# Optimization experiments

Measured on AMD Instinct MI355X. Metric: run time of the kernel, lower is better.

Reference implementation:

```python
import jax, jax.numpy as jnp
import numpy as np
from jax import lax

VOC = 32000; H = 512; T = 256; B = 64; L = 2; MAXLEN = 32; SOS = 1


def setup_inputs() -> dict:
    key = jax.random.key(0)
    ks = jax.random.split(key, 20)
    s = 1.0 / np.sqrt(H)
    u = lambda k, shape: jax.random.uniform(k, shape, jnp.float32, -s, s)
    inp = {}
    inp["input"] = jax.random.randint(ks[0], (T, B), 0, VOC)
    inp["emb_enc"] = jax.random.normal(ks[1], (VOC, H), jnp.float32) * 0.1
    inp["emb_dec"] = jax.random.normal(ks[2], (VOC, H), jnp.float32) * 0.1
    # GRU weights, torch layout: W_ih (3H, in), W_hh (3H, H), biases (3H,); stacked over layers
    inp["enc_Wih"] = u(ks[3], (L, 3 * H, H)); inp["enc_Whh"] = u(ks[4], (L, 3 * H, H))
    inp["enc_bih"] = u(ks[5], (L, 3 * H));   inp["enc_bhh"] = u(ks[6], (L, 3 * H))
    inp["dec_Wih"] = u(ks[7], (L, 3 * H, H)); inp["dec_Whh"] = u(ks[8], (L, 3 * H, H))
    inp["dec_bih"] = u(ks[9], (L, 3 * H));   inp["dec_bhh"] = u(ks[10], (L, 3 * H))
    inp["attn_W"] = u(ks[11], (T, (L + 1) * H)); inp["attn_b"] = u(ks[12], (T,))
    inp["comb_W"] = u(ks[13], (H, 2 * H));       inp["comb_b"] = u(ks[14], (H,))
    inp["avg_W"] = u(ks[15], (1, H))   # dueling value head, no bias
    inp["adv_W"] = u(ks[16], (VOC, H)) # dueling advantage head, no bias
    return inp


def _gru_cell(x, h, Wih, Whh, bih, bhh):
    gi = x @ Wih.T + bih
    gh = h @ Whh.T + bhh
    ir, iz, in_ = jnp.split(gi, 3, axis=-1)
    hr, hz, hn = jnp.split(gh, 3, axis=-1)
    r = jax.nn.sigmoid(ir + hr)
    z = jax.nn.sigmoid(iz + hz)
    n = jnp.tanh(in_ + r * hn)
    return (1.0 - z) * n + z * h


def _gru_step(x, h, Wih, Whh, bih, bhh):
    # x: (B,H), h: (L,B,H) -> new h (L,B,H), top-layer output (B,H)
    hs = []
    for l in range(L):
        hl = _gru_cell(x, h[l], Wih[l], Whh[l], bih[l], bhh[l])
        hs.append(hl)
        x = hl
    return jnp.stack(hs), x


def _forward(input, emb_enc, emb_dec, enc_Wih, enc_Whh, enc_bih, enc_bhh,
             dec_Wih, dec_Whh, dec_bih, dec_bhh, attn_W, attn_b,
             comb_W, comb_b, avg_W, adv_W):
    # ----- encoder -----
    emb = jax.nn.relu(emb_enc[input])  # (T,B,H)
    h0 = jnp.zeros((L, B, H), jnp.float32)

    def enc_step(h, x):
        h2, top = _gru_step(x, h, enc_Wih, enc_Whh, enc_bih, enc_bhh)
        return h2, top

    states, gru_out = lax.scan(enc_step, h0, emb)  # gru_out: (T,B,H)

    def dec_step(carry, _):
        h, word = carry
        e = jax.nn.relu(emb_dec[word])                       # (B,H)
        sv = jnp.reshape(h, (B, L * H))                      # matches torch .view(-1,1,L*H)
        a = jax.nn.relu(jnp.concatenate([e, sv], -1) @ attn_W.T + attn_b)  # (B,T)
        applied = jnp.einsum('bt,tbh->bh', a, gru_out)       # (B,H)
        comb = jax.nn.relu(jnp.concatenate([e, applied], -1) @ comb_W.T + comb_b)
        h2, top = _gru_step(comb, h, dec_Wih, dec_Whh, dec_bih, dec_bhh)
        values = top @ avg_W.T + top @ adv_W.T               # (B,1)+(B,VOC) -> (B,VOC)
        word2 = jnp.argmax(values, axis=-1)
        q = jnp.take_along_axis(values, word2[:, None], axis=-1)[:, 0]
        return (h2, word2), (top, q)

    word0 = jnp.full((B,), SOS, dtype=jnp.int32)
    _, (tops, qs) = lax.scan(dec_step, (states, word0), None, length=MAXLEN)
    sentences = tops[:, None]  # (MAXLEN,1,B,H) mirrors stacking (1,B,H) rnn_outs
    return sentences, qs       # qs: (MAXLEN,B)


def reference(input, emb_enc, emb_dec, enc_Wih, enc_Whh, enc_bih, enc_bhh,
              dec_Wih, dec_Whh, dec_bih, dec_bhh, attn_W, attn_b,
              comb_W, comb_b, avg_W, adv_W):
    return _forward(input, emb_enc, emb_dec, enc_Wih, enc_Whh, enc_bih, enc_bhh,
                    dec_Wih, dec_Whh, dec_bih, dec_bhh, attn_W, attn_b,
                    comb_W, comb_b, avg_W, adv_W)
```

## Files before the change

### kernel.cpp

```cpp
#include <hip/hip_runtime.h>
#include <math.h>

#define VOCN 32000
#define HN 512
#define TN 256
#define BN 64
#define MAXLENN 32
#define SOSW 1

#define WS_FLAG     0
#define WS_REL      8192
#define WS_H        8448
#define WS_WORD     (WS_H + 131072)
#define WS_A        (WS_WORD + 64)
#define WS_APPLIED  (WS_A + 16384)
#define WS_COMB     (WS_APPLIED + 32768)
#define WS_PVAL     (WS_COMB + 32768)
#define WS_PIDX     (WS_PVAL + 16384)
#define WS_GRUOUT   (WS_PIDX + 16384)
#define WS_ZERO_BYTES ((WS_H + 131072) * 4)

typedef float f4 __attribute__((ext_vector_type(4)));

__device__ __forceinline__ f4 ld4(const float* p) { return *(const f4*)p; }
__device__ __forceinline__ float dot4(f4 a, f4 b, float acc) {
  acc = fmaf(a.x, b.x, acc); acc = fmaf(a.y, b.y, acc);
  acc = fmaf(a.z, b.z, acc); acc = fmaf(a.w, b.w, acc); return acc;
}
__device__ __forceinline__ f4 relu4(f4 v) {
  v.x = fmaxf(v.x, 0.f); v.y = fmaxf(v.y, 0.f);
  v.z = fmaxf(v.z, 0.f); v.w = fmaxf(v.w, 0.f); return v;
}
__device__ __forceinline__ float sigmoidf_(float x) { return 1.f / (1.f + expf(-x)); }

__device__ __forceinline__ float ldcg(const float* p) {
  float v;
  asm volatile("global_load_dword %0, %1, off sc0 sc1\n\ts_waitcnt vmcnt(0)"
               : "=&v"(v) : "v"(p) : "memory");
  return v;
}
__device__ __forceinline__ int ldcg_i(const int* p) {
  int v;
  asm volatile("global_load_dword %0, %1, off sc0 sc1\n\ts_waitcnt vmcnt(0)"
               : "=&v"(v) : "v"(p) : "memory");
  return v;
}
__device__ __forceinline__ void stcg(float* p, float v) {
  asm volatile("global_store_dword %0, %1, off sc0 sc1" :: "v"(p), "v"(v) : "memory");
}
__device__ __forceinline__ void stcg_i(int* p, int v) {
  asm volatile("global_store_dword %0, %1, off sc0 sc1" :: "v"(p), "v"(v) : "memory");
}
__device__ __forceinline__ void ldcg_b4(const float* p0, const float* p1,
                                        const float* p2, const float* p3,
                                        f4& v0, f4& v1, f4& v2, f4& v3) {
  asm volatile(
      "global_load_dwordx4 %0, %4, off sc0 sc1\n\t"
      "global_load_dwordx4 %1, %5, off sc0 sc1\n\t"
      "global_load_dwordx4 %2, %6, off sc0 sc1\n\t"
      "global_load_dwordx4 %3, %7, off sc0 sc1\n\t"
      "s_waitcnt vmcnt(0)"
      : "=&v"(v0), "=&v"(v1), "=&v"(v2), "=&v"(v3)
      : "v"(p0), "v"(p1), "v"(p2), "v"(p3)
      : "memory");
}
__device__ __forceinline__ void ldcg_b8(const float* p0, const float* p1,
    const float* p2, const float* p3, const float* p4, const float* p5,
    const float* p6, const float* p7,
    f4& v0, f4& v1, f4& v2, f4& v3, f4& v4, f4& v5, f4& v6, f4& v7) {
  asm volatile(
      "global_load_dwordx4 %0, %8, off sc0 sc1\n\t"
      "global_load_dwordx4 %1, %9, off sc0 sc1\n\t"
      "global_load_dwordx4 %2, %10, off sc0 sc1\n\t"
      "global_load_dwordx4 %3, %11, off sc0 sc1\n\t"
      "global_load_dwordx4 %4, %12, off sc0 sc1\n\t"
      "global_load_dwordx4 %5, %13, off sc0 sc1\n\t"
      "global_load_dwordx4 %6, %14, off sc0 sc1\n\t"
      "global_load_dwordx4 %7, %15, off sc0 sc1\n\t"
      "s_waitcnt vmcnt(0)"
      : "=&v"(v0), "=&v"(v1), "=&v"(v2), "=&v"(v3),
        "=&v"(v4), "=&v"(v5), "=&v"(v6), "=&v"(v7)
      : "v"(p0), "v"(p1), "v"(p2), "v"(p3), "v"(p4), "v"(p5), "v"(p6), "v"(p7)
      : "memory");
}
__device__ __forceinline__ void ldcg_row8(const float* p, f4 (&v)[8]) {
  asm volatile(
      "global_load_dwordx4 %0, %8, off sc0 sc1\n\t"
      "global_load_dwordx4 %1, %8, off offset:16 sc0 sc1\n\t"
      "global_load_dwordx4 %2, %8, off offset:32 sc0 sc1\n\t"
      "global_load_dwordx4 %3, %8, off offset:48 sc0 sc1\n\t"
      "global_load_dwordx4 %4, %8, off offset:64 sc0 sc1\n\t"
      "global_load_dwordx4 %5, %8, off offset:80 sc0 sc1\n\t"
      "global_load_dwordx4 %6, %8, off offset:96 sc0 sc1\n\t"
      "global_load_dwordx4 %7, %8, off offset:112 sc0 sc1\n\t"
      "s_waitcnt vmcnt(0)"
      : "=&v"(v[0]), "=&v"(v[1]), "=&v"(v[2]), "=&v"(v[3]),
        "=&v"(v[4]), "=&v"(v[5]), "=&v"(v[6]), "=&v"(v[7])
      : "v"(p)
      : "memory");
}

__device__ __forceinline__ void grid_barrier(int* wsi, int gen) {
  asm volatile("s_waitcnt vmcnt(0) lgkmcnt(0)" ::: "memory");
  __syncthreads();
  const int bid = blockIdx.x;
  const int tid = threadIdx.x;
  if (bid == 0) {
    if (tid == 0)
      __hip_atomic_store(wsi + WS_FLAG, gen, __ATOMIC_RELAXED, __HIP_MEMORY_SCOPE_AGENT);
    int* fp = wsi + WS_FLAG + tid * 32;
    for (;;) {
      int v = __hip_atomic_load(fp, __ATOMIC_RELAXED, __HIP_MEMORY_SCOPE_AGENT);
      if (__syncthreads_and(v >= gen)) break;
      __builtin_amdgcn_s_sleep(2);
    }
    if (tid < 8)
      __hip_atomic_store(wsi + WS_REL + tid * 16, gen, __ATOMIC_RELAXED, __HIP_MEMORY_SCOPE_AGENT);
    __syncthreads();
  } else {
    if (tid == 0) {
      __hip_atomic_store(wsi + WS_FLAG + bid * 32, gen, __ATOMIC_RELAXED, __HIP_MEMORY_SCOPE_AGENT);
      int* rp = wsi + WS_REL + (bid & 7) * 16;
      while (__hip_atomic_load(rp, __ATOMIC_RELAXED, __HIP_MEMORY_SCOPE_AGENT) < gen)
        __builtin_amdgcn_s_sleep(2);
    }
    __syncthreads();
  }
}

__device__ __forceinline__ void gru_phase(
    const float* __restrict__ x_base, const int* __restrict__ tok,
    const float* __restrict__ h_rows,
    const float* __restrict__ Wih, const float* __restrict__ Whh,
    const float* __restrict__ bih, const float* __restrict__ bhh,
    float* __restrict__ h_out, float* __restrict__ aux_out,
    int rb, float* lds)
{
  const int tid = threadIdx.x;
  const int bg = rb >> 6;
  const int jg = rb & 63;
  f4* x4l = (f4*)lds;
  f4* h4l = ((f4*)lds) + 1024;

  const float* xp[4]; const float* hp[4]; int loff[4];
#pragma unroll
  for (int i = 0; i < 4; ++i) {
    int tau = tid + (i << 8);
    int b = tau >> 5;
    int kq = tau & 31;
    int gb = bg * 32 + b;
    const float* xr = tok ? (x_base + (size_t)tok[gb] * HN) : (x_base + (size_t)gb * HN);
    xp[i] = xr + (kq << 2);
    hp[i] = h_rows + (size_t)gb * HN + (kq << 2);
    loff[i] = (b << 5) + (kq ^ (b & 7));
  }
  const bool cachedx = (tok != nullptr);
  f4 pxv[4], phv[4];
  if (cachedx) {
#pragma unroll
    for (int i = 0; i < 4; ++i) pxv[i] = ld4(xp[i]);
    ldcg_b4(hp[0], hp[1], hp[2], hp[3], phv[0], phv[1], phv[2], phv[3]);
  } else {
    ldcg_b8(xp[0], xp[1], xp[2], xp[3], hp[0], hp[1], hp[2], hp[3],
            pxv[0], pxv[1], pxv[2], pxv[3], phv[0], phv[1], phv[2], phv[3]);
  }

  const int bl = tid & 31;
  const int jl = tid >> 5;
  const int j = (jg << 3) + jl;
  const float* wi0 = Wih + (size_t)j * HN;
  const float* wi1 = Wih + (size_t)(512 + j) * HN;
  const float* wi2 = Wih + (size_t)(1024 + j) * HN;
  const float* wh0 = Whh + (size_t)j * HN;
  const float* wh1 = Whh + (size_t)(512 + j) * HN;
  const float* wh2 = Whh + (size_t)(1024 + j) * HN;
  float ax0 = 0.f, ax1 = 0.f, ax2 = 0.f, ah0 = 0.f, ah1 = 0.f, ah2 = 0.f;
  const int rdbase = bl << 5;
  const int rdx = bl & 7;

#pragma unroll 1
  for (int ch = 0; ch < 4; ++ch) {
    __syncthreads();
#pragma unroll
    for (int i = 0; i < 4; ++i) {
      x4l[loff[i]] = cachedx ? relu4(pxv[i]) : pxv[i];
      h4l[loff[i]] = phv[i];
    }
    __syncthreads();
    if (ch < 3) {
      const int off = (ch + 1) * 128;
      if (cachedx) {
#pragma unroll
        for (int i = 0; i < 4; ++i) pxv[i] = ld4(xp[i] + off);
        ldcg_b4(hp[0] + off, hp[1] + off, hp[2] + off, hp[3] + off,
                phv[0], phv[1], phv[2], phv[3]);
      } else {
        ldcg_b8(xp[0] + off, xp[1] + off, xp[2] + off, xp[3] + off,
                hp[0] + off, hp[1] + off, hp[2] + off, hp[3] + off,
                pxv[0], pxv[1], pxv[2], pxv[3], phv[0], phv[1], phv[2], phv[3]);
      }
    }
    const int k0 = ch << 7;
#pragma unroll 4
    for (int kq = 0; kq < 32; ++kq) {
      f4 xv = x4l[rdbase + (kq ^ rdx)];
      f4 hv = h4l[rdbase + (kq ^ rdx)];
      const int kk = k0 + (kq << 2);
      ax0 = dot4(xv, ld4(wi0 + kk), ax0);
      ah0 = dot4(hv, ld4(wh0 + kk), ah0);
      ax1 = dot4(xv, ld4(wi1 + kk), ax1);
      ah1 = dot4(hv, ld4(wh1 + kk), ah1);
      ax2 = dot4(xv, ld4(wi2 + kk), ax2);
      ah2 = dot4(hv, ld4(wh2 + kk), ah2);
    }
  }
  const int gb = bg * 32 + bl;
  const float hold = ldcg(h_rows + (size_t)gb * HN + j);
  const float r = sigmoidf_(ax0 + bih[j] + ah0 + bhh[j]);
  const float z = sigmoidf_(ax1 + bih[512 + j] + ah1 + bhh[512 + j]);
  const float n = tanhf(ax2 + bih[1024 + j] + r * (ah2 + bhh[1024 + j]));
  const float hv = (1.f - z) * n + z * hold;
  stcg(h_out + (size_t)gb * HN + j, hv);
  if (aux_out) stcg(aux_out + (size_t)gb * HN + j, hv);
}

__device__ __forceinline__ void d1_attn(
    const float* __restrict__ emb_dec, const int* __restrict__ word_buf, int s,
    const float* __restrict__ hflat, const float* __restrict__ attn_W,
    const float* __restrict__ attn_b, float* __restrict__ a_buf, int bid, float* lds)
{
  const int tid = threadIdx.x;
  const int b = tid & 63, q = tid >> 6;
  int wb = (s == 0) ? SOSW : ldcg_i(word_buf + b);
  wb = wb < 0 ? 0 : (wb > VOCN - 1 ? VOCN - 1 : wb);
  const float* er = emb_dec + (size_t)wb * HN;
  const float* hr = hflat + b * 1024;
  const float* wr = attn_W + (size_t)bid * 1536;
  float acc = 0.f;
  const int kbeg = q * 384, kend = kbeg + 384;
  int k = kbeg;
  const int kc = (kend < 512) ? kend : 512;
  for (; k < kc; k += 4)
    acc = dot4(relu4(ld4(er + k)), ld4(wr + k), acc);
  if (k < 512) k = 512;
  for (; k < kend; k += 32) {
    f4 hv[8]; ldcg_row8(hr + (k - 512), hv);
#pragma unroll
    for (int jq = 0; jq < 8; ++jq)
      acc = dot4(hv[jq], ld4(wr + k + (jq << 2)), acc);
  }
  lds[(b << 2) + q] = acc;
  __syncthreads();
  if (tid < 64) {
    float v = lds[tid * 4] + lds[tid * 4 + 1] + lds[tid * 4 + 2] + lds[tid * 4 + 3];
    v += attn_b[bid];
    stcg(a_buf + tid * 256 + bid, fmaxf(v, 0.f));
  }
}

__device__ __forceinline__ void d2_applied(const float* __restrict__ a_buf,
    const float* __restrict__ gru_out, float* __restrict__ applied, int bid, float* lds)
{
  const int tid = threadIdx.x;
  const int b = bid & 63, hc = bid >> 6;
  f4* al4 = (f4*)lds;
  float* al = lds;
  float* red = lds + 256;
  if (tid < 64) {
    f4 av;
    const float* p = a_buf + b * 256 + (tid << 2);
    asm volatile("global_load_dwordx4 %0, %1, off sc0 sc1\n\ts_waitcnt vmcnt(0)"
                 : "=&v"(av) : "v"(p) : "memory");
    al4[tid] = av;
  }
  __syncthreads();
  const int hl = tid & 127, th = tid >> 7;
  const int hh = (hc << 7) + hl;
  const float* gp = gru_out + (size_t)b * HN + hh;
  float acc = 0.f;
  const int t0 = th << 7;
#pragma unroll 4
  for (int t = t0; t < t0 + 128; ++t)
    acc = fmaf(al[t], gp[(size_t)t * (BN * HN)], acc);
  red[tid] = acc;
  __syncthreads();
  if (tid < 128)
    stcg(applied + (size_t)b * HN + (hc << 7) + tid, red[tid] + red[tid + 128]);
}

__device__ __forceinline__ void d3_comb(const float* __restrict__ emb_dec,
    const int* __restrict__ word_buf, int s, const float* __restrict__ applied,
    const float* __restrict__ comb_W, const float* __restrict__ comb_b,
    float* __restrict__ comb, int bid, float* lds)
{
  const int tid = threadIdx.x;
  const int b = tid & 63, q = tid >> 6;
  int wb = (s == 0) ? SOSW : ldcg_i(word_buf + b);
  wb = wb < 0 ? 0 : (wb > VOCN - 1 ? VOCN - 1 : wb);
  const float* er = emb_dec + (size_t)wb * HN;
  const float* apr = applied + (size_t)b * HN;
#pragma unroll
  for (int cc = 0; cc < 2; ++cc) {
    const int col = (bid << 1) + cc;
    const float* wr = comb_W + (size_t)col * 1024;
    float acc = 0.f;
    const int kbeg = q << 8, kend = kbeg + 256;
    int k = kbeg;
    const int kc = (kend < 512) ? kend : 512;
    for (; k < kc; k += 4)
      acc = dot4(relu4(ld4(er + k)), ld4(wr + k), acc);
    if (k < 512) k = 512;
    for (; k < kend; k += 32) {
      f4 av[8]; ldcg_row8(apr + (k - 512), av);
#pragma unroll
      for (int jq = 0; jq < 8; ++jq)
        acc = dot4(av[jq], ld4(wr + k + (jq << 2)), acc);
    }
    lds[cc * 256 + (b << 2) + q] = acc;
  }
  __syncthreads();
  if (tid < 128) {
    const int cc = tid >> 6, b2 = tid & 63;
    const int col = (bid << 1) + cc;
    float v = lds[cc * 256 + b2 * 4] + lds[cc * 256 + b2 * 4 + 1] +
              lds[cc * 256 + b2 * 4 + 2] + lds[cc * 256 + b2 * 4 + 3];
    v += comb_b[col];
    stcg(comb + (size_t)b2 * HN + col, fmaxf(v, 0.f));
  }
}

__device__ __forceinline__ void d6_values(const float* __restrict__ top,
    const float* __restrict__ adv_W, float* __restrict__ pval, int* __restrict__ pidx,
    int bid, float* lds)
{
  const int tid = threadIdx.x;
  const int c0 = bid * 125;
  f4* tl = (f4*)lds;
  f4* wl = ((f4*)lds) + 2048;
  float* sval = lds + 12288;
  int* sidx = (int*)(lds + 12288 + 256);

  const float* tp[8]; int loff[8];
#pragma unroll
  for (int i = 0; i < 8; ++i) {
    int tau = tid + (i << 8);
    int b = tau >> 5, kq = tau & 31;
    tp[i] = top + b * HN + (kq << 2);
    loff[i] = (b << 5) + (kq ^ (b & 7));
  }
  f4 pv[8];
  ldcg_b8(tp[0], tp[1], tp[2], tp[3], tp[4], tp[5], tp[6], tp[7],
          pv[0], pv[1], pv[2], pv[3], pv[4], pv[5], pv[6], pv[7]);

  const int bl = tid & 63;
  const int cq = tid >> 6;
  const int rdbase = bl << 5;
  const int rdx = bl & 7;

  float acc[32];
#pragma unroll
  for (int i = 0; i < 32; ++i) acc[i] = 0.f;

#pragma unroll 1
  for (int ch = 0; ch < 4; ++ch) {
    __syncthreads();
#pragma unroll
    for (int i = 0; i < 8; ++i) tl[loff[i]] = pv[i];
    __syncthreads();
    if (ch < 3) {
      const int off = (ch + 1) * 128;
      ldcg_b8(tp[0] + off, tp[1] + off, tp[2] + off, tp[3] + off,
              tp[4] + off, tp[5] + off, tp[6] + off, tp[7] + off,
              pv[0], pv[1], pv[2], pv[3], pv[4], pv[5], pv[6], pv[7]);
    }
#pragma unroll 1
    for (int cg = 0; cg < 4; ++cg) {
#pragma unroll
      for (int r = 0; r < 4; ++r) {
        const int qq = tid + (r << 8);
        int c = c0 + (cg << 5) + (qq >> 5);
        if (c > VOCN - 1) c = VOCN - 1;
        wl[qq] = ld4(adv_W + (size_t)c * HN + (ch << 7) + ((qq & 31) << 2));
      }
      __syncthreads();
      const int wbase = cq << 8;
#pragma unroll 4
      for (int kq = 0; kq < 32; ++kq) {
        f4 tv = tl[rdbase + (kq ^ rdx)];
        const int wq = wbase + kq;
        acc[(cg << 3) + 0] = dot4(tv, wl[wq +   0], acc[(cg << 3) + 0]);
        acc[(cg << 3) + 1] = dot4(tv, wl[wq +  32], acc[(cg << 3) + 1]);
        acc[(cg << 3) + 2] = dot4(tv, wl[wq +  64], acc[(cg << 3) + 2]);
        acc[(cg << 3) + 3] = dot4(tv, wl[wq +  96], acc[(cg << 3) + 3]);
        acc[(cg << 3) + 4] = dot4(tv, wl[wq + 128], acc[(cg << 3) + 4]);
        acc[(cg << 3) + 5] = dot4(tv, wl[wq + 160], acc[(cg << 3) + 5]);
        acc[(cg << 3) + 6] = dot4(tv, wl[wq + 192], acc[(cg << 3) + 6]);
        acc[(cg << 3) + 7] = dot4(tv, wl[wq + 224], acc[(cg << 3) + 7]);
      }
      __syncthreads();
    }
  }
  float bv = -3.4e38f; int bi = 2147483647;
#pragma unroll
  for (int i = 0; i < 32; ++i) {
    const int cl = ((i >> 3) << 5) + (cq << 3) + (i & 7);
    if (cl < 125) {
      float v = acc[i];
      if (v > bv) { bv = v; bi = c0 + cl; }
    }
  }
  sval[(bl << 2) + cq] = bv;
  sidx[(bl << 2) + cq] = bi;
  __syncthreads();
  if (tid < 64) {
    float v = sval[tid << 2]; int ii = sidx[tid << 2];
#pragma unroll
    for (int h2 = 1; h2 < 4; ++h2) {
      float v2 = sval[(tid << 2) + h2]; int i2 = sidx[(tid << 2) + h2];
      if (v2 > v || (v2 == v && i2 < ii)) { v = v2; ii = i2; }
    }
    stcg(pval + tid * 256 + bid, v);
    stcg_i(pidx + tid * 256 + bid, ii);
  }
}

__device__ __forceinline__ void d7_reduce(const float* __restrict__ top,
    const float* __restrict__ avg_W, const float* __restrict__ pval,
    const int* __restrict__ pidx, float* __restrict__ qs_out,
    int* __restrict__ word_buf, float* lds)
{
  const int tid = threadIdx.x;
  const int b = tid & 63, q = tid >> 6;
  const float* tr = top + (size_t)b * HN;
  float p = 0.f;
  const int kbeg = q << 7;
#pragma unroll
  for (int bb = 0; bb < 4; ++bb) {
    f4 tv[8]; ldcg_row8(tr + kbeg + bb * 32, tv);
#pragma unroll
    for (int jq = 0; jq < 8; ++jq)
      p = dot4(tv[jq], ld4(avg_W + kbeg + bb * 32 + (jq << 2)), p);
  }
  float* av = lds;
  float* avl = lds + 256;
  float* rv = lds + 320;
  int* ri = (int*)(lds + 576);
  av[(b << 2) + q] = p;
  __syncthreads();
  if (tid < 64)
    avl[tid] = av[tid * 4] + av[tid * 4 + 1] + av[tid * 4 + 2] + av[tid * 4 + 3];
  float bv = -3.4e38f; int bi = 2147483647;
  const float* pvr = pval + b * 256 + (q << 6);
  const float* pir = (const float*)(pidx) + b * 256 + (q << 6);
#pragma unroll
  for (int bb = 0; bb < 2; ++bb) {
    f4 v4[8], i4[8];
    ldcg_row8(pvr + bb * 32, v4);
    ldcg_row8(pir + bb * 32, i4);
#pragma unroll
    for (int jq = 0; jq < 8; ++jq) {
      float vv[4] = { v4[jq].x, v4[jq].y, v4[jq].z, v4[jq].w };
      int iv[4] = { __float_as_int(i4[jq].x), __float_as_int(i4[jq].y),
                    __float_as_int(i4[jq].z), __float_as_int(i4[jq].w) };
#pragma unroll
      for (int c = 0; c < 4; ++c) {
        if (vv[c] > bv || (vv[c] == bv && iv[c] < bi)) { bv = vv[c]; bi = iv[c]; }
      }
    }
  }
  rv[(b << 2) + q] = bv;
  ri[(b << 2) + q] = bi;
  __syncthreads();
  if (tid < 64) {
    float v = rv[tid << 2]; int ii = ri[tid << 2];
#pragma unroll
    for (int k = 1; k < 4; ++k) {
      float v2 = rv[(tid << 2) + k]; int i2 = ri[(tid << 2) + k];
      if (v2 > v || (v2 == v && i2 < ii)) { v = v2; ii = i2; }
    }
    qs_out[tid] = v + avl[tid];
    stcg_i(word_buf + tid, ii);
  }
}

__global__ void __launch_bounds__(256)
seq2seq_kernel(const int* __restrict__ input, const float* __restrict__ emb_enc,
               const float* __restrict__ emb_dec,
               const float* __restrict__ enc_Wih, const float* __restrict__ enc_Whh,
               const float* __restrict__ enc_bih, const float* __restrict__ enc_bhh,
               const float* __restrict__ dec_Wih, const float* __restrict__ dec_Whh,
               const float* __restrict__ dec_bih, const float* __restrict__ dec_bhh,
               const float* __restrict__ attn_W, const float* __restrict__ attn_b,
               const float* __restrict__ comb_W, const float* __restrict__ comb_b,
               const float* __restrict__ avg_W, const float* __restrict__ adv_W,
               float* __restrict__ out, float* __restrict__ ws)
{
  __shared__ float lds[12800];
  const int bid = blockIdx.x;
  int* wsi = (int*)ws;
  float* hbuf = ws + WS_H;
  int* word_buf = (int*)(ws + WS_WORD);
  float* a_buf = ws + WS_A;
  float* applied = ws + WS_APPLIED;
  float* comb = ws + WS_COMB;
  float* pval = ws + WS_PVAL;
  int* pidx = (int*)(ws + WS_PIDX);
  float* gru_out = ws + WS_GRUOUT;
  int gen = 0;

#pragma unroll 1
  for (int p = 0; p <= 256; ++p) {
    if (bid < 128) {
      if (p < 256) {
        const int t = p;
        gru_phase(emb_enc, input + t * BN,
                  hbuf + (size_t)(t & 1) * 65536,
                  enc_Wih, enc_Whh, enc_bih, enc_bhh,
                  hbuf + (size_t)((t + 1) & 1) * 65536,
                  nullptr, bid, lds);
      }
    } else {
      if (p >= 1) {
        const int t = p - 1;
        gru_phase(hbuf + (size_t)((t + 1) & 1) * 65536, nullptr,
                  hbuf + (size_t)(t & 1) * 65536 + 32768,
                  enc_Wih + 786432, enc_Whh + 786432,
                  enc_bih + 1536, enc_bhh + 1536,
                  hbuf + (size_t)((t + 1) & 1) * 65536 + 32768,
                  gru_out + (size_t)t * (BN * HN), bid - 128, lds);
      }
    }
    grid_barrier(wsi, ++gen);
  }

  __threadfence();

#pragma unroll 1
  for (int s = 0; s < 32; ++s) {
    const float* hflat = hbuf + (size_t)(s & 1) * 65536;
    float* hnew = hbuf + (size_t)((s + 1) & 1) * 65536;

    d1_attn(emb_dec, word_buf, s, hflat, attn_W, attn_b, a_buf, bid, lds);
    grid_barrier(wsi, ++gen);

    d2_applied(a_buf, gru_out, applied, bid, lds);
    grid_barrier(wsi, ++gen);

    d3_comb(emb_dec, word_buf, s, applied, comb_W, comb_b, comb, bid, lds);
    grid_barrier(wsi, ++gen);

    if (bid < 128)
      gru_phase(comb, nullptr, hflat, dec_Wih, dec_Whh, dec_bih, dec_bhh,
                hnew, nullptr, bid, lds);
    grid_barrier(wsi, ++gen);

    if (bid < 128)
      gru_phase(hnew, nullptr, hflat + 32768,
                dec_Wih + 786432, dec_Whh + 786432, dec_bih + 1536, dec_bhh + 1536,
                hnew + 32768, out + (size_t)s * (BN * HN), bid, lds);
    grid_barrier(wsi, ++gen);

    d6_values(hnew + 32768, adv_W, pval, pidx, bid, lds);
    grid_barrier(wsi, ++gen);

    if (bid == 0)
      d7_reduce(hnew + 32768, avg_W, pval, pidx,
                out + (size_t)MAXLENN * BN * HN + s * BN, word_buf, lds);
    grid_barrier(wsi, ++gen);
  }
}

extern "C" void kernel_launch(void* const* d_in, const int* in_sizes, int n_in,
                              void* d_out, int out_size, void* d_ws, size_t ws_size,
                              hipStream_t stream) {
  (void)in_sizes; (void)n_in; (void)out_size; (void)ws_size;
  const int* input      = (const int*)d_in[0];
  const float* emb_enc  = (const float*)d_in[1];
  const float* emb_dec  = (const float*)d_in[2];
  const float* enc_Wih  = (const float*)d_in[3];
  const float* enc_Whh  = (const float*)d_in[4];
  const float* enc_bih  = (const float*)d_in[5];
  const float* enc_bhh  = (const float*)d_in[6];
  const float* dec_Wih  = (const float*)d_in[7];
  const float* dec_Whh  = (const float*)d_in[8];
  const float* dec_bih  = (const float*)d_in[9];
  const float* dec_bhh  = (const float*)d_in[10];
  const float* attn_W   = (const float*)d_in[11];
  const float* attn_b   = (const float*)d_in[12];
  const float* comb_W   = (const float*)d_in[13];
  const float* comb_b   = (const float*)d_in[14];
  const float* avg_W    = (const float*)d_in[15];
  const float* adv_W    = (const float*)d_in[16];
  float* out = (float*)d_out;
  float* ws  = (float*)d_ws;

  hipMemsetAsync(d_ws, 0, WS_ZERO_BYTES, stream);

  seq2seq_kernel<<<dim3(256), dim3(256), 0, stream>>>(
      input, emb_enc, emb_dec, enc_Wih, enc_Whh, enc_bih, enc_bhh,
      dec_Wih, dec_Whh, dec_bih, dec_bhh, attn_W, attn_b,
      comb_W, comb_b, avg_W, adv_W, out, ws);
}
```

Before: 21.47 ms.

## Replace argmax reduce phase with packed 64-bit atomic max and double block size

Drops the separate single-block argmax reduction phase and its grid barrier. Each decoder step's per-block argmax is now merged through a 64-bit atomic max on order-preserving float keys with an inverted index for ties, and the word and q-value are decoded in the next step. Blocks grow to 512 threads, so the GRU phases run on half as many blocks with two batch groups each, and the attention, applied, comb and value phases are reorganised for the wider block, with the avg-head dot moved into block 0 of the value phase. This cuts 32 grid barriers and a serial reduction, at the cost of global atomics, larger LDS use and possible occupancy changes.

```diff
diff --git a/kernel.cpp b/kernel.cpp
--- a/kernel.cpp
+++ b/kernel.cpp
@@ -11,14 +11,13 @@
 #define WS_FLAG     0
 #define WS_REL      8192
 #define WS_H        8448
-#define WS_WORD     (WS_H + 131072)
-#define WS_A        (WS_WORD + 64)
+#define WS_CELLS    (WS_H + 131072)
+#define WS_AVG      (WS_CELLS + 4096)
+#define WS_A        (WS_AVG + 64)
 #define WS_APPLIED  (WS_A + 16384)
 #define WS_COMB     (WS_APPLIED + 32768)
-#define WS_PVAL     (WS_COMB + 32768)
-#define WS_PIDX     (WS_PVAL + 16384)
-#define WS_GRUOUT   (WS_PIDX + 16384)
-#define WS_ZERO_BYTES ((WS_H + 131072) * 4)
+#define WS_GRUOUT   (WS_COMB + 32768)
+#define WS_ZERO_BYTES ((WS_CELLS + 4096) * 4)
 
 typedef float f4 __attribute__((ext_vector_type(4)));
 
@@ -39,16 +38,7 @@
                : "=&v"(v) : "v"(p) : "memory");
   return v;
 }
-__device__ __forceinline__ int ldcg_i(const int* p) {
-  int v;
-  asm volatile("global_load_dword %0, %1, off sc0 sc1\n\ts_waitcnt vmcnt(0)"
-               : "=&v"(v) : "v"(p) : "memory");
-  return v;
-}
 __device__ __forceinline__ void stcg(float* p, float v) {
-  asm volatile("global_store_dword %0, %1, off sc0 sc1" :: "v"(p), "v"(v) : "memory");
-}
-__device__ __forceinline__ void stcg_i(int* p, int v) {
   asm volatile("global_store_dword %0, %1, off sc0 sc1" :: "v"(p), "v"(v) : "memory");
 }
 __device__ __forceinline__ void ldcg_b4(const float* p0, const float* p1,
@@ -108,9 +98,11 @@
   if (bid == 0) {
     if (tid == 0)
       __hip_atomic_store(wsi + WS_FLAG, gen, __ATOMIC_RELAXED, __HIP_MEMORY_SCOPE_AGENT);
-    int* fp = wsi + WS_FLAG + tid * 32;
+    int* fp = wsi + WS_FLAG + (tid & 255) * 32;
     for (;;) {
-      int v = __hip_atomic_load(fp, __ATOMIC_RELAXED, __HIP_MEMORY_SCOPE_AGENT);
+      int v = gen;
+      if (tid < 256)
+        v = __hip_atomic_load(fp, __ATOMIC_RELAXED, __HIP_MEMORY_SCOPE_AGENT);
       if (__syncthreads_and(v >= gen)) break;
       __builtin_amdgcn_s_sleep(2);
     }
@@ -128,24 +120,39 @@
   }
 }
 
+__device__ __forceinline__ unsigned ord_enc(float v) {
+  unsigned u = __float_as_uint(v);
+  return (u & 0x80000000u) ? ~u : (u | 0x80000000u);
+}
+__device__ __forceinline__ float ord_dec(unsigned k32) {
+  unsigned u = (k32 & 0x80000000u) ? (k32 ^ 0x80000000u) : ~k32;
+  return __uint_as_float(u);
+}
+__device__ __forceinline__ int decode_word(const unsigned long long* cell) {
+  unsigned long long key = __hip_atomic_load(cell, __ATOMIC_RELAXED,
+                                             __HIP_MEMORY_SCOPE_AGENT);
+  int wb = (int)(0xFFFFFFFFu - (unsigned)(key & 0xFFFFFFFFull));
+  return wb < 0 ? 0 : (wb > VOCN - 1 ? VOCN - 1 : wb);
+}
+
 __device__ __forceinline__ void gru_phase(
     const float* __restrict__ x_base, const int* __restrict__ tok,
     const float* __restrict__ h_rows,
     const float* __restrict__ Wih, const float* __restrict__ Whh,
     const float* __restrict__ bih, const float* __restrict__ bhh,
     float* __restrict__ h_out, float* __restrict__ aux_out,
-    int rb, float* lds)
+    int jg, float* lds)
 {
   const int tid = threadIdx.x;
-  const int bg = rb >> 6;
-  const int jg = rb & 63;
-  f4* x4l = (f4*)lds;
-  f4* h4l = ((f4*)lds) + 1024;
+  const int tid2 = tid & 255;
+  const int bg = tid >> 8;
+  f4* x4l = (f4*)lds + (bg << 11);
+  f4* h4l = x4l + 1024;
 
   const float* xp[4]; const float* hp[4]; int loff[4];
 #pragma unroll
   for (int i = 0; i < 4; ++i) {
-    int tau = tid + (i << 8);
+    int tau = tid2 + (i << 8);
     int b = tau >> 5;
     int kq = tau & 31;
     int gb = bg * 32 + b;
@@ -165,8 +172,8 @@
             pxv[0], pxv[1], pxv[2], pxv[3], phv[0], phv[1], phv[2], phv[3]);
   }
 
-  const int bl = tid & 31;
-  const int jl = tid >> 5;
+  const int bl = tid2 & 31;
+  const int jl = tid2 >> 5;
   const int j = (jg << 3) + jl;
   const float* wi0 = Wih + (size_t)j * HN;
   const float* wi1 = Wih + (size_t)(512 + j) * HN;
@@ -225,19 +232,29 @@
 }
 
 __device__ __forceinline__ void d1_attn(
-    const float* __restrict__ emb_dec, const int* __restrict__ word_buf, int s,
-    const float* __restrict__ hflat, const float* __restrict__ attn_W,
-    const float* __restrict__ attn_b, float* __restrict__ a_buf, int bid, float* lds)
+    const float* __restrict__ emb_dec, const unsigned long long* __restrict__ cells,
+    int s, const float* __restrict__ hflat, const float* __restrict__ attn_W,
+    const float* __restrict__ attn_b, float* __restrict__ a_buf,
+    const float* __restrict__ avg_buf, float* __restrict__ qs_base,
+    int bid, float* lds)
 {
   const int tid = threadIdx.x;
   const int b = tid & 63, q = tid >> 6;
-  int wb = (s == 0) ? SOSW : ldcg_i(word_buf + b);
-  wb = wb < 0 ? 0 : (wb > VOCN - 1 ? VOCN - 1 : wb);
+  int* wlds = (int*)(lds + 576);
+  if (s > 0 && tid < 64)
+    wlds[tid] = decode_word(cells + (size_t)(s - 1) * 64 + tid);
+  if (s > 0 && bid == 0 && tid < 64) {
+    unsigned long long key = __hip_atomic_load(cells + (size_t)(s - 1) * 64 + tid,
+                                               __ATOMIC_RELAXED, __HIP_MEMORY_SCOPE_AGENT);
+    qs_base[(size_t)(s - 1) * BN + tid] = ord_dec((unsigned)(key >> 32)) + ldcg(avg_buf + tid);
+  }
+  __syncthreads();
+  const int wb = (s == 0) ? SOSW : wlds[b];
   const float* er = emb_dec + (size_t)wb * HN;
   const float* hr = hflat + b * 1024;
   const float* wr = attn_W + (size_t)bid * 1536;
   float acc = 0.f;
-  const int kbeg = q * 384, kend = kbeg + 384;
+  const int kbeg = q * 192, kend = kbeg + 192;
   int k = kbeg;
   const int kc = (kend < 512) ? kend : 512;
   for (; k < kc; k += 4)
@@ -249,10 +266,13 @@
     for (int jq = 0; jq < 8; ++jq)
       acc = dot4(hv[jq], ld4(wr + k + (jq << 2)), acc);
   }
-  lds[(b << 2) + q] = acc;
+  __syncthreads();
+  lds[(b << 3) + q] = acc;
   __syncthreads();
   if (tid < 64) {
-    float v = lds[tid * 4] + lds[tid * 4 + 1] + lds[tid * 4 + 2] + lds[tid * 4 + 3];
+    float v = 0.f;
+#pragma unroll
+    for (int i = 0; i < 8; ++i) v += lds[(tid << 3) + i];
     v += attn_b[bid];
     stcg(a_buf + tid * 256 + bid, fmaxf(v, 0.f));
   }
@@ -278,212 +298,172 @@
   const int hh = (hc << 7) + hl;
   const float* gp = gru_out + (size_t)b * HN + hh;
   float acc = 0.f;
-  const int t0 = th << 7;
+  const int t0 = th << 6;
 #pragma unroll 4
-  for (int t = t0; t < t0 + 128; ++t)
+  for (int t = t0; t < t0 + 64; ++t)
     acc = fmaf(al[t], gp[(size_t)t * (BN * HN)], acc);
   red[tid] = acc;
   __syncthreads();
   if (tid < 128)
-    stcg(applied + (size_t)b * HN + (hc << 7) + tid, red[tid] + red[tid + 128]);
+    stcg(applied + (size_t)b * HN + (hc << 7) + tid,
+         red[tid] + red[tid + 128] + red[tid + 256] + red[tid + 384]);
 }
 
 __device__ __forceinline__ void d3_comb(const float* __restrict__ emb_dec,
-    const int* __restrict__ word_buf, int s, const float* __restrict__ applied,
-    const float* __restrict__ comb_W, const float* __restrict__ comb_b,
-    float* __restrict__ comb, int bid, float* lds)
+    const unsigned long long* __restrict__ cells, int s,
+    const float* __restrict__ applied, const float* __restrict__ comb_W,
+    const float* __restrict__ comb_b, float* __restrict__ comb, int bid, float* lds)
 {
   const int tid = threadIdx.x;
   const int b = tid & 63, q = tid >> 6;
-  int wb = (s == 0) ? SOSW : ldcg_i(word_buf + b);
-  wb = wb < 0 ? 0 : (wb > VOCN - 1 ? VOCN - 1 : wb);
+  int* wlds = (int*)(lds + 1088);
+  if (s > 0 && tid < 64)
+    wlds[tid] = decode_word(cells + (size_t)(s - 1) * 64 + tid);
+  __syncthreads();
+  const int wb = (s == 0) ? SOSW : wlds[b];
   const float* er = emb_dec + (size_t)wb * HN;
   const float* apr = applied + (size_t)b * HN;
-#pragma unroll
-  for (int cc = 0; cc < 2; ++cc) {
-    const int col = (bid << 1) + cc;
-    const float* wr = comb_W + (size_t)col * 1024;
-    float acc = 0.f;
-    const int kbeg = q << 8, kend = kbeg + 256;
-    int k = kbeg;
-    const int kc = (kend < 512) ? kend : 512;
-    for (; k < kc; k += 4)
-      acc = dot4(relu4(ld4(er + k)), ld4(wr + k), acc);
-    if (k < 512) k = 512;
-    for (; k < kend; k += 32) {
-      f4 av[8]; ldcg_row8(apr + (k - 512), av);
-#pragma unroll
-      for (int jq = 0; jq < 8; ++jq)
-        acc = dot4(av[jq], ld4(wr + k + (jq << 2)), acc);
-    }
-    lds[cc * 256 + (b << 2) + q] = acc;
-  }
+  const int col0 = bid << 1;
+  const float* w0 = comb_W + (size_t)col0 * 1024;
+  const float* w1 = w0 + 1024;
+  float a0 = 0.f, a1 = 0.f;
+  const int kb = q << 7;
+  if (q < 4) {
+    for (int k = kb; k < kb + 128; k += 4) {
+      f4 e = relu4(ld4(er + k));
+      a0 = dot4(e, ld4(w0 + k), a0);
+      a1 = dot4(e, ld4(w1 + k), a1);
+    }
+  } else {
+#pragma unroll 1
+    for (int r = 0; r < 4; ++r) {
+      f4 av[8]; ldcg_row8(apr + (kb - 512) + (r << 5), av);
+#pragma unroll
+      for (int jq = 0; jq < 8; ++jq) {
+        a0 = dot4(av[jq], ld4(w0 + kb + (r << 5) + (jq << 2)), a0);
+        a1 = dot4(av[jq], ld4(w1 + kb + (r << 5) + (jq << 2)), a1);
+      }
+    }
+  }
+  __syncthreads();
+  lds[(b << 3) + q] = a0;
+  lds[512 + (b << 3) + q] = a1;
   __syncthreads();
   if (tid < 128) {
     const int cc = tid >> 6, b2 = tid & 63;
-    const int col = (bid << 1) + cc;
-    float v = lds[cc * 256 + b2 * 4] + lds[cc * 256 + b2 * 4 + 1] +
-              lds[cc * 256 + b2 * 4 + 2] + lds[cc * 256 + b2 * 4 + 3];
-    v += comb_b[col];
-    stcg(comb + (size_t)b2 * HN + col, fmaxf(v, 0.f));
+    const float* base = lds + cc * 512;
+    float v = 0.f;
+#pragma unroll
+    for (int i = 0; i < 8; ++i) v += base[(b2 << 3) + i];
+    v += comb_b[col0 + cc];
+    stcg(comb + (size_t)b2 * HN + col0 + cc, fmaxf(v, 0.f));
   }
 }
 
 __device__ __forceinline__ void d6_values(const float* __restrict__ top,
-    const float* __restrict__ adv_W, float* __restrict__ pval, int* __restrict__ pidx,
+    const float* __restrict__ adv_W, const float* __restrict__ avg_W,
+    unsigned long long* __restrict__ cellsS, float* __restrict__ avg_buf,
     int bid, float* lds)
 {
   const int tid = threadIdx.x;
   const int c0 = bid * 125;
   f4* tl = (f4*)lds;
   f4* wl = ((f4*)lds) + 2048;
-  float* sval = lds + 12288;
-  int* sidx = (int*)(lds + 12288 + 256);
-
-  const float* tp[8]; int loff[8];
-#pragma unroll
-  for (int i = 0; i < 8; ++i) {
-    int tau = tid + (i << 8);
+
+  const float* tp[4]; int loff[4];
+#pragma unroll
+  for (int i = 0; i < 4; ++i) {
+    int tau = tid + (i << 9);
     int b = tau >> 5, kq = tau & 31;
     tp[i] = top + b * HN + (kq << 2);
     loff[i] = (b << 5) + (kq ^ (b & 7));
   }
-  f4 pv[8];
-  ldcg_b8(tp[0], tp[1], tp[2], tp[3], tp[4], tp[5], tp[6], tp[7],
-          pv[0], pv[1], pv[2], pv[3], pv[4], pv[5], pv[6], pv[7]);
-
-  const int bl = tid & 63;
-  const int cq = tid >> 6;
-  const int rdbase = bl << 5;
-  const int rdx = bl & 7;
-
-  float acc[32];
-#pragma unroll
-  for (int i = 0; i < 32; ++i) acc[i] = 0.f;
+  f4 pv[4];
+  ldcg_b4(tp[0], tp[1], tp[2], tp[3], pv[0], pv[1], pv[2], pv[3]);
+
+  const int rp = tid >> 4;
+  const int co = tid & 15;
+  const int r0 = rp << 1;
+  float acc0[8], acc1[8];
+#pragma unroll
+  for (int i = 0; i < 8; ++i) { acc0[i] = 0.f; acc1[i] = 0.f; }
+  float avgacc = 0.f;
 
 #pragma unroll 1
   for (int ch = 0; ch < 4; ++ch) {
     __syncthreads();
 #pragma unroll
-    for (int i = 0; i < 8; ++i) tl[loff[i]] = pv[i];
+    for (int i = 0; i < 4; ++i) tl[loff[i]] = pv[i];
     __syncthreads();
     if (ch < 3) {
       const int off = (ch + 1) * 128;
-      ldcg_b8(tp[0] + off, tp[1] + off, tp[2] + off, tp[3] + off,
-              tp[4] + off, tp[5] + off, tp[6] + off, tp[7] + off,
-              pv[0], pv[1], pv[2], pv[3], pv[4], pv[5], pv[6], pv[7]);
+      ldcg_b4(tp[0] + off, tp[1] + off, tp[2] + off, tp[3] + off,
+              pv[0], pv[1], pv[2], pv[3]);
+    }
+    if (bid == 0 && tid < 64) {
+#pragma unroll 4
+      for (int kq = 0; kq < 32; ++kq)
+        avgacc = dot4(tl[(tid << 5) + (kq ^ (tid & 7))],
+                      ld4(avg_W + (ch << 7) + (kq << 2)), avgacc);
     }
 #pragma unroll 1
-    for (int cg = 0; cg < 4; ++cg) {
+    for (int w = 0; w < 2; ++w) {
 #pragma unroll
       for (int r = 0; r < 4; ++r) {
-        const int qq = tid + (r << 8);
-        int c = c0 + (cg << 5) + (qq >> 5);
-        if (c > VOCN - 1) c = VOCN - 1;
-        wl[qq] = ld4(adv_W + (size_t)c * HN + (ch << 7) + ((qq & 31) << 2));
+        const int qq = tid + (r << 9);
+        const int cl = qq >> 4, kql = qq & 15;
+        int c = c0 + cl; if (c > VOCN - 1) c = VOCN - 1;
+        wl[(cl << 4) + (kql ^ ((cl >> 3) & 7))] =
+            ld4(adv_W + (size_t)c * HN + (ch << 7) + (w << 6) + (kql << 2));
       }
       __syncthreads();
-      const int wbase = cq << 8;
-#pragma unroll 4
-      for (int kq = 0; kq < 32; ++kq) {
-        f4 tv = tl[rdbase + (kq ^ rdx)];
-        const int wq = wbase + kq;
-        acc[(cg << 3) + 0] = dot4(tv, wl[wq +   0], acc[(cg << 3) + 0]);
-        acc[(cg << 3) + 1] = dot4(tv, wl[wq +  32], acc[(cg << 3) + 1]);
-        acc[(cg << 3) + 2] = dot4(tv, wl[wq +  64], acc[(cg << 3) + 2]);
-        acc[(cg << 3) + 3] = dot4(tv, wl[wq +  96], acc[(cg << 3) + 3]);
-        acc[(cg << 3) + 4] = dot4(tv, wl[wq + 128], acc[(cg << 3) + 4]);
-        acc[(cg << 3) + 5] = dot4(tv, wl[wq + 160], acc[(cg << 3) + 5]);
-        acc[(cg << 3) + 6] = dot4(tv, wl[wq + 192], acc[(cg << 3) + 6]);
-        acc[(cg << 3) + 7] = dot4(tv, wl[wq + 224], acc[(cg << 3) + 7]);
+      const int kqb = w << 4;
+#pragma unroll 2
+      for (int kql = 0; kql < 16; ++kql) {
+        const int kq = kqb + kql;
+        f4 t0 = tl[(r0 << 5) + (kq ^ (r0 & 7))];
+        f4 t1 = tl[((r0 + 1) << 5) + (kq ^ ((r0 + 1) & 7))];
+#pragma unroll
+        for (int j = 0; j < 8; ++j) {
+          const int cl = (co << 3) + j;
+          f4 wv = wl[(cl << 4) + (kql ^ ((cl >> 3) & 7))];
+          acc0[j] = dot4(t0, wv, acc0[j]);
+          acc1[j] = dot4(t1, wv, acc1[j]);
+        }
       }
       __syncthreads();
     }
   }
-  float bv = -3.4e38f; int bi = 2147483647;
-#pragma unroll
-  for (int i = 0; i < 32; ++i) {
-    const int cl = ((i >> 3) << 5) + (cq << 3) + (i & 7);
+  float bv0 = -3.4e38f, bv1 = -3.4e38f; int bi0 = 2147483647, bi1 = 2147483647;
+#pragma unroll
+  for (int j = 0; j < 8; ++j) {
+    const int cl = (co << 3) + j;
     if (cl < 125) {
-      float v = acc[i];
-      if (v > bv) { bv = v; bi = c0 + cl; }
-    }
-  }
-  sval[(bl << 2) + cq] = bv;
-  sidx[(bl << 2) + cq] = bi;
+      if (acc0[j] > bv0) { bv0 = acc0[j]; bi0 = c0 + cl; }
+      if (acc1[j] > bv1) { bv1 = acc1[j]; bi1 = c0 + cl; }
+    }
+  }
+  float* sval = lds;
+  int* sidx = (int*)(lds + 1024);
+  sval[(r0 << 4) + co] = bv0;  sidx[(r0 << 4) + co] = bi0;
+  sval[((r0 + 1) << 4) + co] = bv1;  sidx[((r0 + 1) << 4) + co] = bi1;
   __syncthreads();
   if (tid < 64) {
-    float v = sval[tid << 2]; int ii = sidx[tid << 2];
-#pragma unroll
-    for (int h2 = 1; h2 < 4; ++h2) {
-      float v2 = sval[(tid << 2) + h2]; int i2 = sidx[(tid << 2) + h2];
+    float v = sval[tid << 4]; int ii = sidx[tid << 4];
+#pragma unroll
+    for (int h2 = 1; h2 < 16; ++h2) {
+      float v2 = sval[(tid << 4) + h2]; int i2 = sidx[(tid << 4) + h2];
       if (v2 > v || (v2 == v && i2 < ii)) { v = v2; ii = i2; }
     }
-    stcg(pval + tid * 256 + bid, v);
-    stcg_i(pidx + tid * 256 + bid, ii);
-  }
-}
-
-__device__ __forceinline__ void d7_reduce(const float* __restrict__ top,
-    const float* __restrict__ avg_W, const float* __restrict__ pval,
-    const int* __restrict__ pidx, float* __restrict__ qs_out,
-    int* __restrict__ word_buf, float* lds)
-{
-  const int tid = threadIdx.x;
-  const int b = tid & 63, q = tid >> 6;
-  const float* tr = top + (size_t)b * HN;
-  float p = 0.f;
-  const int kbeg = q << 7;
-#pragma unroll
-  for (int bb = 0; bb < 4; ++bb) {
-    f4 tv[8]; ldcg_row8(tr + kbeg + bb * 32, tv);
-#pragma unroll
-    for (int jq = 0; jq < 8; ++jq)
-      p = dot4(tv[jq], ld4(avg_W + kbeg + bb * 32 + (jq << 2)), p);
-  }
-  float* av = lds;
-  float* avl = lds + 256;
-  float* rv = lds + 320;
-  int* ri = (int*)(lds + 576);
-  av[(b << 2) + q] = p;
-  __syncthreads();
-  if (tid < 64)
-    avl[tid] = av[tid * 4] + av[tid * 4 + 1] + av[tid * 4 + 2] + av[tid * 4 + 3];
-  float bv = -3.4e38f; int bi = 2147483647;
-  const float* pvr = pval + b * 256 + (q << 6);
-  const float* pir = (const float*)(pidx) + b * 256 + (q << 6);
-#pragma unroll
-  for (int bb = 0; bb < 2; ++bb) {
-    f4 v4[8], i4[8];
-    ldcg_row8(pvr + bb * 32, v4);
-    ldcg_row8(pir + bb * 32, i4);
-#pragma unroll
-    for (int jq = 0; jq < 8; ++jq) {
-      float vv[4] = { v4[jq].x, v4[jq].y, v4[jq].z, v4[jq].w };
-      int iv[4] = { __float_as_int(i4[jq].x), __float_as_int(i4[jq].y),
-                    __float_as_int(i4[jq].z), __float_as_int(i4[jq].w) };
-#pragma unroll
-      for (int c = 0; c < 4; ++c) {
-        if (vv[c] > bv || (vv[c] == bv && iv[c] < bi)) { bv = vv[c]; bi = iv[c]; }
-      }
-    }
-  }
-  rv[(b << 2) + q] = bv;
-  ri[(b << 2) + q] = bi;
-  __syncthreads();
-  if (tid < 64) {
-    float v = rv[tid << 2]; int ii = ri[tid << 2];
-#pragma unroll
-    for (int k = 1; k < 4; ++k) {
-      float v2 = rv[(tid << 2) + k]; int i2 = ri[(tid << 2) + k];
-      if (v2 > v || (v2 == v && i2 < ii)) { v = v2; ii = i2; }
-    }
-    qs_out[tid] = v + avl[tid];
-    stcg_i(word_buf + tid, ii);
-  }
-}
-
-__global__ void __launch_bounds__(256)
+    unsigned long long key = ((unsigned long long)ord_enc(v) << 32) |
+                             (unsigned long long)(0xFFFFFFFFu - (unsigned)ii);
+    __hip_atomic_fetch_max(cellsS + tid, key, __ATOMIC_RELAXED,
+                           __HIP_MEMORY_SCOPE_AGENT);
+  }
+  if (bid == 0 && tid < 64) stcg(avg_buf + tid, avgacc);
+}
+
+__global__ void __launch_bounds__(512)
 seq2seq_kernel(const int* __restrict__ input, const float* __restrict__ emb_enc,
                const float* __restrict__ emb_dec,
                const float* __restrict__ enc_Wih, const float* __restrict__ enc_Whh,
@@ -495,31 +475,30 @@
                const float* __restrict__ avg_W, const float* __restrict__ adv_W,
                float* __restrict__ out, float* __restrict__ ws)
 {
-  __shared__ float lds[12800];
+  __shared__ float lds[16384];
   const int bid = blockIdx.x;
   int* wsi = (int*)ws;
   float* hbuf = ws + WS_H;
-  int* word_buf = (int*)(ws + WS_WORD);
+  unsigned long long* cells = (unsigned long long*)(ws + WS_CELLS);
+  float* avg_buf = ws + WS_AVG;
   float* a_buf = ws + WS_A;
   float* applied = ws + WS_APPLIED;
   float* comb = ws + WS_COMB;
-  float* pval = ws + WS_PVAL;
-  int* pidx = (int*)(ws + WS_PIDX);
   float* gru_out = ws + WS_GRUOUT;
+  float* qs_base = out + (size_t)MAXLENN * BN * HN;
   int gen = 0;
 
 #pragma unroll 1
   for (int p = 0; p <= 256; ++p) {
-    if (bid < 128) {
+    if (bid < 64) {
       if (p < 256) {
-        const int t = p;
-        gru_phase(emb_enc, input + t * BN,
-                  hbuf + (size_t)(t & 1) * 65536,
+        gru_phase(emb_enc, input + p * BN,
+                  hbuf + (size_t)(p & 1) * 65536,
                   enc_Wih, enc_Whh, enc_bih, enc_bhh,
-                  hbuf + (size_t)((t + 1) & 1) * 65536,
+                  hbuf + (size_t)((p + 1) & 1) * 65536,
                   nullptr, bid, lds);
       }
-    } else {
+    } else if (bid < 128) {
       if (p >= 1) {
         const int t = p - 1;
         gru_phase(hbuf + (size_t)((t + 1) & 1) * 65536, nullptr,
@@ -527,7 +506,7 @@
                   enc_Wih + 786432, enc_Whh + 786432,
                   enc_bih + 1536, enc_bhh + 1536,
                   hbuf + (size_t)((t + 1) & 1) * 65536 + 32768,
-                  gru_out + (size_t)t * (BN * HN), bid - 128, lds);
+                  gru_out + (size_t)t * (BN * HN), bid - 64, lds);
       }
     }
     grid_barrier(wsi, ++gen);
@@ -540,33 +519,35 @@
     const float* hflat = hbuf + (size_t)(s & 1) * 65536;
     float* hnew = hbuf + (size_t)((s + 1) & 1) * 65536;
 
-    d1_attn(emb_dec, word_buf, s, hflat, attn_W, attn_b, a_buf, bid, lds);
+    d1_attn(emb_dec, cells, s, hflat, attn_W, attn_b, a_buf, avg_buf, qs_base, bid, lds);
     grid_barrier(wsi, ++gen);
 
     d2_applied(a_buf, gru_out, applied, bid, lds);
     grid_barrier(wsi, ++gen);
 
-    d3_comb(emb_dec, word_buf, s, applied, comb_W, comb_b, comb, bid, lds);
-    grid_barrier(wsi, ++gen);
-
-    if (bid < 128)
+    d3_comb(emb_dec, cells, s, applied, comb_W, comb_b, comb, bid, lds);
+    grid_barrier(wsi, ++gen);
+
+    if (bid < 64)
       gru_phase(comb, nullptr, hflat, dec_Wih, dec_Whh, dec_bih, dec_bhh,
                 hnew, nullptr, bid, lds);
     grid_barrier(wsi, ++gen);
 
-    if (bid < 128)
+    if (bid < 64)
       gru_phase(hnew, nullptr, hflat + 32768,
                 dec_Wih + 786432, dec_Whh + 786432, dec_bih + 1536, dec_bhh + 1536,
                 hnew + 32768, out + (size_t)s * (BN * HN), bid, lds);
     grid_barrier(wsi, ++gen);
 
-    d6_values(hnew + 32768, adv_W, pval, pidx, bid, lds);
-    grid_barrier(wsi, ++gen);
-
-    if (bid == 0)
-      d7_reduce(hnew + 32768, avg_W, pval, pidx,
-                out + (size_t)MAXLENN * BN * HN + s * BN, word_buf, lds);
-    grid_barrier(wsi, ++gen);
+    d6_values(hnew + 32768, adv_W, avg_W, cells + (size_t)s * 64, avg_buf, bid, lds);
+    grid_barrier(wsi, ++gen);
+  }
+
+  if (bid == 0 && threadIdx.x < 64) {
+    const int tid = threadIdx.x;
+    unsigned long long key = __hip_atomic_load(cells + (size_t)31 * 64 + tid,
+                                               __ATOMIC_RELAXED, __HIP_MEMORY_SCOPE_AGENT);
+    qs_base[(size_t)31 * BN + tid] = ord_dec((unsigned)(key >> 32)) + ldcg(avg_buf + tid);
   }
 }
 
@@ -596,7 +577,7 @@
 
   hipMemsetAsync(d_ws, 0, WS_ZERO_BYTES, stream);
 
-  seq2seq_kernel<<<dim3(256), dim3(256), 0, stream>>>(
+  seq2seq_kernel<<<dim3(256), dim3(512), 0, stream>>>(
       input, emb_enc, emb_dec, enc_Wih, enc_Whh, enc_bih, enc_bhh,
       dec_Wih, dec_Whh, dec_bih, dec_bhh, attn_W, attn_b,
       comb_W, comb_b, avg_W, adv_W, out, ws);
```

Result: no change. 21.76 ms (+1.4%).
